# Kernel optimization log

Measured on AMD Instinct MI355X. Metric: run time of the kernel, lower is better.

Reference implementation:

```python
import jax, jax.numpy as jnp
import numpy as np

N_VOXELS = 200000
DIM = 96
KVOL = 343  # 7^3 depthwise kernel offsets
N_EDGES = 3200000


def setup_inputs() -> dict:
    key = jax.random.key(0)
    ks = jax.random.split(key, 10)
    feats = jax.random.normal(ks[0], (N_VOXELS, DIM), dtype=jnp.float32)
    w_dw = jax.random.normal(ks[1], (KVOL, DIM), dtype=jnp.float32) * 0.02
    b_dw = jax.random.normal(ks[2], (DIM,), dtype=jnp.float32) * 0.02
    ln_w = jnp.ones((DIM,), dtype=jnp.float32)
    ln_b = jnp.zeros((DIM,), dtype=jnp.float32)
    w1 = jax.random.normal(ks[3], (DIM, 4 * DIM), dtype=jnp.float32) * 0.02
    b1 = jax.random.normal(ks[4], (4 * DIM,), dtype=jnp.float32) * 0.02
    w2 = jax.random.normal(ks[5], (4 * DIM, DIM), dtype=jnp.float32) * 0.02
    b2 = jax.random.normal(ks[6], (DIM,), dtype=jnp.float32) * 0.02
    in_idx = jax.random.randint(ks[7], (N_EDGES,), 0, N_VOXELS, dtype=jnp.int32)
    out_idx = jax.random.randint(ks[8], (N_EDGES,), 0, N_VOXELS, dtype=jnp.int32)
    kernel_idx = jax.random.randint(ks[9], (N_EDGES,), 0, KVOL, dtype=jnp.int32)
    return {"feats": feats, "w_dw": w_dw, "b_dw": b_dw, "ln_w": ln_w,
            "ln_b": ln_b, "w1": w1, "b1": b1, "w2": w2, "b2": b2,
            "in_idx": in_idx, "out_idx": out_idx, "kernel_idx": kernel_idx}


def reference(feats, w_dw, b_dw, ln_w, ln_b, w1, b1, w2, b2,
              in_idx, out_idx, kernel_idx):
    n = feats.shape[0]
    # sparse depthwise conv via kernel-map gather/scatter:
    # out[o, c] += feats[i, c] * w_dw[k, c] for each edge (i, o, k)
    contrib = feats[in_idx] * w_dw[kernel_idx]           # [E, C]
    x = jax.ops.segment_sum(contrib, out_idx, num_segments=n) + b_dw
    # LayerNorm over channels, eps=1e-6
    mu = jnp.mean(x, axis=-1, keepdims=True)
    var = jnp.mean(jnp.square(x - mu), axis=-1, keepdims=True)
    x = (x - mu) * jax.lax.rsqrt(var + 1e-6) * ln_w + ln_b
    # pointwise MLP with exact GELU
    h = jax.nn.gelu(x @ w1 + b1, approximate=False)      # [N, 4C]
    x = h @ w2 + b2                                      # [N, C]
    # residual (drop_path rate 0.0 -> identity)
    return feats + x
```

## Files before the change

### kernel.cpp

```cpp
#include <hip/hip_runtime.h>
#include <hip/hip_bf16.h>

#define NVOX 200000
#define DIM 96
#define KVOL 343
#define NEDGE 3200000
#define HID 384
#define TM 32
#define SLOT_CAP 48
#define CSTR 16

typedef __attribute__((ext_vector_type(8))) __bf16 bf16x8;
typedef __attribute__((ext_vector_type(4))) __bf16 bf16x4;
typedef __attribute__((ext_vector_type(4))) float f32x4;
typedef __attribute__((ext_vector_type(4))) int i32x4;

__global__ void prep(const float* __restrict__ feats, const float* __restrict__ w1,
                     const float* __restrict__ w2, const float* __restrict__ w_dw,
                     __bf16* __restrict__ featsb, __hip_bfloat16* __restrict__ w1t,
                     __hip_bfloat16* __restrict__ w2t, __bf16* __restrict__ wdwb,
                     int* __restrict__ cnt) {
    int t = blockIdx.x * 256 + threadIdx.x;
    f32x4 v = __builtin_nontemporal_load((const f32x4*)(feats + t * 4));
    bf16x4 o;
    o[0] = (__bf16)v.x; o[1] = (__bf16)v.y; o[2] = (__bf16)v.z; o[3] = (__bf16)v.w;
    __builtin_nontemporal_store(o, (bf16x4*)(featsb + t * 4));
    if (t < HID * DIM) {
        int n1 = t / DIM, k1 = t % DIM;
        w1t[t] = __float2bfloat16(w1[k1 * HID + n1]);
        int n2 = t / HID, k2 = t % HID;
        w2t[t] = __float2bfloat16(w2[k2 * DIM + n2]);
        if (t < KVOL * DIM) wdwb[t] = (__bf16)w_dw[t];
    }
    if (t < NVOX) cnt[t * CSTR] = 0;
}

__global__ void scatter_T(const i32x4* __restrict__ in4, const i32x4* __restrict__ out4,
                          const i32x4* __restrict__ k4, int* __restrict__ cnt,
                          unsigned* __restrict__ slots) {
    int t = blockIdx.x * 256 + threadIdx.x;
    i32x4 i = __builtin_nontemporal_load(&in4[t]);
    i32x4 o = __builtin_nontemporal_load(&out4[t]);
    i32x4 k = __builtin_nontemporal_load(&k4[t]);
    int d;
    d = atomicAdd(&cnt[o.x * CSTR], 1);
    if (d < SLOT_CAP) slots[d * NVOX + o.x] = (unsigned)i.x | ((unsigned)k.x << 18);
    d = atomicAdd(&cnt[o.y * CSTR], 1);
    if (d < SLOT_CAP) slots[d * NVOX + o.y] = (unsigned)i.y | ((unsigned)k.y << 18);
    d = atomicAdd(&cnt[o.z * CSTR], 1);
    if (d < SLOT_CAP) slots[d * NVOX + o.z] = (unsigned)i.z | ((unsigned)k.z << 18);
    d = atomicAdd(&cnt[o.w * CSTR], 1);
    if (d < SLOT_CAP) slots[d * NVOX + o.w] = (unsigned)i.w | ((unsigned)k.w << 18);
}

__global__ __launch_bounds__(256, 4) void fused_all(
    const __bf16* __restrict__ featsb, const __bf16* __restrict__ wdwb,
    const float* __restrict__ b_dw,
    const float* __restrict__ ln_w, const float* __restrict__ ln_b,
    const __hip_bfloat16* __restrict__ w1t, const float* __restrict__ b1,
    const __hip_bfloat16* __restrict__ w2t, const float* __restrict__ b2,
    const unsigned* __restrict__ slots, const int* __restrict__ cnt,
    float* __restrict__ out)
{
    __shared__ __hip_bfloat16 At[TM][104];
    __shared__ __align__(16) char shb[TM * 200 * 2];
    __hip_bfloat16 (*Ht)[200] = (__hip_bfloat16 (*)[200])shb;
    unsigned (*recsL)[68] = (unsigned (*)[68])shb;

    const int t   = threadIdx.x;
    const int blk = blockIdx.x;

    {
        const int row  = t >> 3;
        const int sub  = t & 7;
        const int part = sub & 3;
        const int half = sub >> 2;
        const int cb   = part * 8;
        const int v    = blk * TM + row;

        int c = cnt[v * CSTR];
        if (c > SLOT_CAP) c = SLOT_CAP;

        for (int d = sub; d < c; d += 8)
            recsL[row][d] = slots[d * NVOX + v];
        __syncthreads();

        float xa[24];
        #pragma unroll
        for (int j = 0; j < 24; ++j) xa[j] = 0.f;

        const __bf16* fbase = featsb + cb;
        const __bf16* wbase = wdwb + cb;
        const unsigned* rl = recsL[row];

        const int e_lo = half ? (c >> 1) : 0;
        const int e_hi = half ? c : (c >> 1);

#define LDE(F, W, ee) { unsigned rr = rl[ee]; \
        const __bf16* fr = fbase + (int)(rr & 0x3FFFFu) * DIM; \
        const __bf16* wr = wbase + (int)(rr >> 18) * DIM; \
        F##0 = *(const bf16x8*)(fr);      W##0 = *(const bf16x8*)(wr); \
        F##1 = *(const bf16x8*)(fr + 32); W##1 = *(const bf16x8*)(wr + 32); \
        F##2 = *(const bf16x8*)(fr + 64); W##2 = *(const bf16x8*)(wr + 64); }

#define ACC(F, W) { \
        _Pragma("unroll") for (int j = 0; j < 8; ++j) xa[j]      += (float)F##0[j] * (float)W##0[j]; \
        _Pragma("unroll") for (int j = 0; j < 8; ++j) xa[8 + j]  += (float)F##1[j] * (float)W##1[j]; \
        _Pragma("unroll") for (int j = 0; j < 8; ++j) xa[16 + j] += (float)F##2[j] * (float)W##2[j]; }

        bf16x8 Af0, Af1, Af2, Aw0, Aw1, Aw2, Bf0, Bf1, Bf2, Bw0, Bw1, Bw2;
        int e = e_lo;
        if (e + 2 <= e_hi) {
            LDE(Af, Aw, e); LDE(Bf, Bw, e + 1);
            e += 2;
            for (; e + 2 <= e_hi; e += 2) {
                bf16x8 Cf0, Cf1, Cf2, Cw0, Cw1, Cw2, Df0, Df1, Df2, Dw0, Dw1, Dw2;
                LDE(Cf, Cw, e); LDE(Df, Dw, e + 1);
                ACC(Af, Aw); ACC(Bf, Bw);
                Af0 = Cf0; Af1 = Cf1; Af2 = Cf2; Aw0 = Cw0; Aw1 = Cw1; Aw2 = Cw2;
                Bf0 = Df0; Bf1 = Df1; Bf2 = Df2; Bw0 = Dw0; Bw1 = Dw1; Bw2 = Dw2;
            }
            ACC(Af, Aw); ACC(Bf, Bw);
        }
        if (e < e_hi) {
            LDE(Af, Aw, e);
            ACC(Af, Aw);
        }
#undef LDE
#undef ACC

        #pragma unroll
        for (int j = 0; j < 24; ++j) xa[j] += __shfl_xor(xa[j], 4);

        float s = 0.f, s2 = 0.f;
        #pragma unroll
        for (int jj = 0; jj < 3; ++jj) {
            #pragma unroll
            for (int j = 0; j < 8; ++j) {
                float x = xa[jj*8+j] + b_dw[jj*32 + cb + j];
                xa[jj*8+j] = x;
                s += x; s2 += x * x;
            }
        }
        s  += __shfl_xor(s, 1);  s  += __shfl_xor(s, 2);
        s2 += __shfl_xor(s2, 1); s2 += __shfl_xor(s2, 2);
        float mean = s * (1.f / 96.f);
        float var  = s2 * (1.f / 96.f) - mean * mean;
        float rstd = rsqrtf(var + 1e-6f);

        if (half == 0) {
            #pragma unroll
            for (int jj = 0; jj < 3; ++jj) {
                bf16x8 pack;
                #pragma unroll
                for (int j = 0; j < 8; ++j) {
                    int cch = jj*32 + cb + j;
                    float xn = (xa[jj*8+j] - mean) * rstd * ln_w[cch] + ln_b[cch];
                    pack[j] = (__bf16)xn;
                }
                *(bf16x8*)&At[row][jj*32 + cb] = pack;
            }
        }
    }
    __syncthreads();

    const int w  = t >> 6;
    const int l  = t & 63;
    const int lr = l & 15;
    const int lk = l >> 4;
    const int rb = w >> 1;
    const int jh = w & 1;

    f32x4 acc2[3];
    #pragma unroll
    for (int j = 0; j < 3; ++j) acc2[j] = (f32x4){0.f, 0.f, 0.f, 0.f};

    #pragma unroll
    for (int h = 0; h < 2; ++h) {
        f32x4 acc[6];
        #pragma unroll
        for (int j = 0; j < 6; ++j) acc[j] = (f32x4){0.f, 0.f, 0.f, 0.f};

        #pragma unroll
        for (int kk = 0; kk < 3; ++kk) {
            bf16x8 a = *(const bf16x8*)&At[rb*16 + lr][kk*32 + lk*8];
            #pragma unroll
            for (int j = 0; j < 6; ++j) {
                int col = h*192 + jh*96 + j*16 + lr;
                bf16x8 b = *(const bf16x8*)&w1t[col * DIM + kk*32 + lk*8];
                acc[j] = __builtin_amdgcn_mfma_f32_16x16x32_bf16(a, b, acc[j], 0, 0, 0);
            }
        }

        if (h == 1) __syncthreads();

        #pragma unroll
        for (int j = 0; j < 6; ++j) {
            int col = h*192 + jh*96 + j*16 + lr;
            float bb = b1[col];
            #pragma unroll
            for (int r = 0; r < 4; ++r) {
                float vv = acc[j][r] + bb;
                float ge = 0.5f * vv * (1.f + erff(vv * 0.70710678f));
                Ht[rb*16 + lk*4 + r][jh*96 + j*16 + lr] = __float2bfloat16(ge);
            }
        }
        __syncthreads();

        #pragma unroll
        for (int kk = 0; kk < 6; ++kk) {
            bf16x8 a = *(const bf16x8*)&Ht[rb*16 + lr][kk*32 + lk*8];
            #pragma unroll
            for (int j = 0; j < 3; ++j) {
                int col = jh*48 + j*16 + lr;
                bf16x8 b = *(const bf16x8*)&w2t[col * HID + (h*6 + kk)*32 + lk*8];
                acc2[j] = __builtin_amdgcn_mfma_f32_16x16x32_bf16(a, b, acc2[j], 0, 0, 0);
            }
        }
    }

    #pragma unroll
    for (int j = 0; j < 3; ++j) {
        int col = jh*48 + j*16 + lr;
        float bb = b2[col];
        #pragma unroll
        for (int r = 0; r < 4; ++r) {
            int grow = blk * TM + rb*16 + lk*4 + r;
            int off = grow * DIM + col;
            float res = (float)featsb[off];
            __builtin_nontemporal_store(acc2[j][r] + bb + res, &out[off]);
        }
    }
}

extern "C" void kernel_launch(void* const* d_in, const int* in_sizes, int n_in,
                              void* d_out, int out_size, void* d_ws, size_t ws_size,
                              hipStream_t stream) {
    const float* feats = (const float*)d_in[0];
    const float* w_dw  = (const float*)d_in[1];
    const float* b_dw  = (const float*)d_in[2];
    const float* ln_w  = (const float*)d_in[3];
    const float* ln_b  = (const float*)d_in[4];
    const float* w1    = (const float*)d_in[5];
    const float* b1    = (const float*)d_in[6];
    const float* w2    = (const float*)d_in[7];
    const float* b2    = (const float*)d_in[8];
    const int* in_idx  = (const int*)d_in[9];
    const int* out_idx = (const int*)d_in[10];
    const int* k_idx   = (const int*)d_in[11];
    float* out = (float*)d_out;

    char* ws = (char*)d_ws;
    unsigned* slots = (unsigned*)ws;
    int* cnt   = (int*)(ws + 38400000);
    __hip_bfloat16* w1t = (__hip_bfloat16*)(ws + 51200000);
    __hip_bfloat16* w2t = (__hip_bfloat16*)(ws + 51273728);
    __bf16* wdwb = (__bf16*)(ws + 51347456);
    __bf16* featsb = (__bf16*)(ws + 51413312);

    prep<<<(NVOX * DIM / 4) / 256, 256, 0, stream>>>(feats, w1, w2, w_dw,
                                                     featsb, w1t, w2t, wdwb, cnt);
    scatter_T<<<NEDGE / 4 / 256, 256, 0, stream>>>((const i32x4*)in_idx,
                                                   (const i32x4*)out_idx,
                                                   (const i32x4*)k_idx, cnt, slots);
    fused_all<<<NVOX / TM, 256, 0, stream>>>(featsb, wdwb, b_dw, ln_w, ln_b,
                                             w1t, b1, w2t, b2, slots, cnt, out);
}
```

Before: 484.9 us.

## Bucket edges per 32-voxel tile and per-XCD sub-bucket to localize scatter atomics

Replaces the per-voxel slot table with per-tile buckets split by XCD ID, packing the in-tile row into the edge record. Each bucket is filled via atomics on a counter local to one XCD, which cuts cross-die atomic traffic and makes the slot writes contiguous. The fused kernel then reads the 8 sub-buckets and regroups records by row in shared memory with LDS atomics. The risks are bucket overflow (capacity 128 per sub-bucket, 48 per row), which silently drops edges, and the extra LDS sort step.

```diff
diff --git a/kernel.cpp b/kernel.cpp
--- a/kernel.cpp
+++ b/kernel.cpp
@@ -7,8 +7,10 @@
 #define NEDGE 3200000
 #define HID 384
 #define TM 32
-#define SLOT_CAP 48
-#define CSTR 16
+#define NBKT (NVOX / TM)
+#define SBCAP 128
+#define ROWCAP 48
+#define XCC_IMM 63508
 
 typedef __attribute__((ext_vector_type(8))) __bf16 bf16x8;
 typedef __attribute__((ext_vector_type(4))) __bf16 bf16x4;
@@ -19,7 +21,7 @@
                      const float* __restrict__ w2, const float* __restrict__ w_dw,
                      __bf16* __restrict__ featsb, __hip_bfloat16* __restrict__ w1t,
                      __hip_bfloat16* __restrict__ w2t, __bf16* __restrict__ wdwb,
-                     int* __restrict__ cnt) {
+                     int* __restrict__ bcnt) {
     int t = blockIdx.x * 256 + threadIdx.x;
     f32x4 v = __builtin_nontemporal_load((const f32x4*)(feats + t * 4));
     bf16x4 o;
@@ -32,25 +34,30 @@
         w2t[t] = __float2bfloat16(w2[k2 * DIM + n2]);
         if (t < KVOL * DIM) wdwb[t] = (__bf16)w_dw[t];
     }
-    if (t < NVOX) cnt[t * CSTR] = 0;
-}
-
-__global__ void scatter_T(const i32x4* __restrict__ in4, const i32x4* __restrict__ out4,
-                          const i32x4* __restrict__ k4, int* __restrict__ cnt,
-                          unsigned* __restrict__ slots) {
+    if (t < NBKT * 8) bcnt[t] = 0;
+}
+
+__global__ void scatter_B(const i32x4* __restrict__ in4, const i32x4* __restrict__ out4,
+                          const i32x4* __restrict__ k4, int* __restrict__ bcnt,
+                          unsigned* __restrict__ sb) {
     int t = blockIdx.x * 256 + threadIdx.x;
+    unsigned xcd = (unsigned)__builtin_amdgcn_s_getreg(XCC_IMM) & 7u;
     i32x4 i = __builtin_nontemporal_load(&in4[t]);
     i32x4 o = __builtin_nontemporal_load(&out4[t]);
     i32x4 k = __builtin_nontemporal_load(&k4[t]);
-    int d;
-    d = atomicAdd(&cnt[o.x * CSTR], 1);
-    if (d < SLOT_CAP) slots[d * NVOX + o.x] = (unsigned)i.x | ((unsigned)k.x << 18);
-    d = atomicAdd(&cnt[o.y * CSTR], 1);
-    if (d < SLOT_CAP) slots[d * NVOX + o.y] = (unsigned)i.y | ((unsigned)k.y << 18);
-    d = atomicAdd(&cnt[o.z * CSTR], 1);
-    if (d < SLOT_CAP) slots[d * NVOX + o.z] = (unsigned)i.z | ((unsigned)k.z << 18);
-    d = atomicAdd(&cnt[o.w * CSTR], 1);
-    if (d < SLOT_CAP) slots[d * NVOX + o.w] = (unsigned)i.w | ((unsigned)k.w << 18);
+    int b, d;
+    b = ((unsigned)o.x >> 5) * 8 + xcd;
+    d = atomicAdd(&bcnt[b], 1);
+    if (d < SBCAP) sb[b * SBCAP + d] = (unsigned)i.x | ((unsigned)k.x << 18) | ((unsigned)(o.x & 31) << 27);
+    b = ((unsigned)o.y >> 5) * 8 + xcd;
+    d = atomicAdd(&bcnt[b], 1);
+    if (d < SBCAP) sb[b * SBCAP + d] = (unsigned)i.y | ((unsigned)k.y << 18) | ((unsigned)(o.y & 31) << 27);
+    b = ((unsigned)o.z >> 5) * 8 + xcd;
+    d = atomicAdd(&bcnt[b], 1);
+    if (d < SBCAP) sb[b * SBCAP + d] = (unsigned)i.z | ((unsigned)k.z << 18) | ((unsigned)(o.z & 31) << 27);
+    b = ((unsigned)o.w >> 5) * 8 + xcd;
+    d = atomicAdd(&bcnt[b], 1);
+    if (d < SBCAP) sb[b * SBCAP + d] = (unsigned)i.w | ((unsigned)k.w << 18) | ((unsigned)(o.w & 31) << 27);
 }
 
 __global__ __launch_bounds__(256, 4) void fused_all(
@@ -59,16 +66,33 @@
     const float* __restrict__ ln_w, const float* __restrict__ ln_b,
     const __hip_bfloat16* __restrict__ w1t, const float* __restrict__ b1,
     const __hip_bfloat16* __restrict__ w2t, const float* __restrict__ b2,
-    const unsigned* __restrict__ slots, const int* __restrict__ cnt,
+    const unsigned* __restrict__ sb, const int* __restrict__ bcnt,
     float* __restrict__ out)
 {
     __shared__ __hip_bfloat16 At[TM][104];
     __shared__ __align__(16) char shb[TM * 200 * 2];
     __hip_bfloat16 (*Ht)[200] = (__hip_bfloat16 (*)[200])shb;
-    unsigned (*recsL)[68] = (unsigned (*)[68])shb;
+    unsigned (*rowlist)[ROWCAP] = (unsigned (*)[ROWCAP])shb;
+    int* rowcnt = (int*)(shb + 32 * ROWCAP * 4);
 
     const int t   = threadIdx.x;
     const int blk = blockIdx.x;
+
+    if (t < 32) rowcnt[t] = 0;
+    __syncthreads();
+    #pragma unroll
+    for (int q = 0; q < 8; ++q) {
+        int cq = bcnt[blk * 8 + q];
+        if (cq > SBCAP) cq = SBCAP;
+        const unsigned* reg = sb + (blk * 8 + q) * SBCAP;
+        for (int i = t; i < cq; i += 256) {
+            unsigned r = reg[i];
+            int row = (int)(r >> 27);
+            int d = atomicAdd(&rowcnt[row], 1);
+            if (d < ROWCAP) rowlist[row][d] = r;
+        }
+    }
+    __syncthreads();
 
     {
         const int row  = t >> 3;
@@ -76,14 +100,9 @@
         const int part = sub & 3;
         const int half = sub >> 2;
         const int cb   = part * 8;
-        const int v    = blk * TM + row;
-
-        int c = cnt[v * CSTR];
-        if (c > SLOT_CAP) c = SLOT_CAP;
-
-        for (int d = sub; d < c; d += 8)
-            recsL[row][d] = slots[d * NVOX + v];
-        __syncthreads();
+
+        int c = rowcnt[row];
+        if (c > ROWCAP) c = ROWCAP;
 
         float xa[24];
         #pragma unroll
@@ -91,14 +110,14 @@
 
         const __bf16* fbase = featsb + cb;
         const __bf16* wbase = wdwb + cb;
-        const unsigned* rl = recsL[row];
+        const unsigned* rl = rowlist[row];
 
         const int e_lo = half ? (c >> 1) : 0;
         const int e_hi = half ? c : (c >> 1);
 
 #define LDE(F, W, ee) { unsigned rr = rl[ee]; \
         const __bf16* fr = fbase + (int)(rr & 0x3FFFFu) * DIM; \
-        const __bf16* wr = wbase + (int)(rr >> 18) * DIM; \
+        const __bf16* wr = wbase + (int)((rr >> 18) & 0x1FFu) * DIM; \
         F##0 = *(const bf16x8*)(fr);      W##0 = *(const bf16x8*)(wr); \
         F##1 = *(const bf16x8*)(fr + 32); W##1 = *(const bf16x8*)(wr + 32); \
         F##2 = *(const bf16x8*)(fr + 64); W##2 = *(const bf16x8*)(wr + 64); }
@@ -251,18 +270,18 @@
     float* out = (float*)d_out;
 
     char* ws = (char*)d_ws;
-    unsigned* slots = (unsigned*)ws;
-    int* cnt   = (int*)(ws + 38400000);
-    __hip_bfloat16* w1t = (__hip_bfloat16*)(ws + 51200000);
-    __hip_bfloat16* w2t = (__hip_bfloat16*)(ws + 51273728);
-    __bf16* wdwb = (__bf16*)(ws + 51347456);
-    __bf16* featsb = (__bf16*)(ws + 51413312);
+    unsigned* sb = (unsigned*)ws;
+    int* bcnt = (int*)(ws + 25600000);
+    __hip_bfloat16* w1t = (__hip_bfloat16*)(ws + 25800000);
+    __hip_bfloat16* w2t = (__hip_bfloat16*)(ws + 25873728);
+    __bf16* wdwb = (__bf16*)(ws + 25947456);
+    __bf16* featsb = (__bf16*)(ws + 26013312);
 
     prep<<<(NVOX * DIM / 4) / 256, 256, 0, stream>>>(feats, w1, w2, w_dw,
-                                                     featsb, w1t, w2t, wdwb, cnt);
-    scatter_T<<<NEDGE / 4 / 256, 256, 0, stream>>>((const i32x4*)in_idx,
+                                                     featsb, w1t, w2t, wdwb, bcnt);
+    scatter_B<<<NEDGE / 4 / 256, 256, 0, stream>>>((const i32x4*)in_idx,
                                                    (const i32x4*)out_idx,
-                                                   (const i32x4*)k_idx, cnt, slots);
-    fused_all<<<NVOX / TM, 256, 0, stream>>>(featsb, wdwb, b_dw, ln_w, ln_b,
-                                             w1t, b1, w2t, b2, slots, cnt, out);
-}
+                                                   (const i32x4*)k_idx, bcnt, sb);
+    fused_all<<<NBKT, 256, 0, stream>>>(featsb, wdwb, b_dw, ln_w, ln_b,
+                                        w1t, b1, w2t, b2, sb, bcnt, out);
+}
```

New measurement: 442.7 us. -8.7%, faster.
